# Kernel optimization log

Hardware: AMD Instinct MI355X
Metric: run time of the kernel (lower is better)

## Reference

```python
import jax, jax.numpy as jnp
import numpy as np

N = 100000   # nodes
E = 800000   # edges
IN = 64      # in_channels
H = 128      # hidden_channels (Embedding_Dimension)
K = 9        # Num_TCN clusters
EPS = 1e-15


def setup_inputs() -> dict:
    key = jax.random.key(0)
    k0, k1, k2, k3, k4 = jax.random.split(key, 5)
    x = jax.random.normal(k0, (N, IN), jnp.float32)
    edge_index = jax.random.randint(k1, (2, E), 0, N, dtype=jnp.int32)
    batch = jnp.zeros((N,), jnp.int32)  # single graph
    W1 = jax.random.normal(k2, (IN, H), jnp.float32) / np.sqrt(IN)
    b1 = jnp.zeros((H,), jnp.float32)
    Wp = jax.random.normal(k3, (H, K), jnp.float32) / np.sqrt(H)
    bp = jax.random.normal(k4, (K,), jnp.float32) * 0.01
    return {"x": x, "edge_index": edge_index, "batch": batch,
            "W1": W1, "b1": b1, "Wp": Wp, "bp": bp}


def gcn_conv(x, edge_index, W, b):
    # GCNConv: h = D^{-1/2} (A + I) D^{-1/2} (x W) + b
    n = x.shape[0]
    h = x @ W  # [N, H]
    loop = jnp.arange(n, dtype=edge_index.dtype)
    row = jnp.concatenate([edge_index[0], loop])  # source
    col = jnp.concatenate([edge_index[1], loop])  # target
    deg = jax.ops.segment_sum(jnp.ones_like(col, jnp.float32), col, n)
    dinv = jax.lax.rsqrt(jnp.maximum(deg, 1.0))  # deg >= 1 (self loops)
    norm = dinv[row] * dinv[col]  # [E+N]
    agg = jax.ops.segment_sum(norm[:, None] * h[row], col, n)  # scatter-add at targets
    return agg + b


def reference(x, edge_index, batch, W1, b1, Wp, bp):
    n = x.shape[0]
    src, dst = edge_index[0], edge_index[1]

    hx = jax.nn.relu(gcn_conv(x, edge_index, W1, b1))  # [N, H]
    s_logits = hx @ Wp + bp                             # [N, K]
    s = jax.nn.softmax(s_logits, axis=-1)

    # pooled features and adjacency: S^T X, S^T A S (A sparse via edge list)
    x_pool = s.T @ hx                                   # [K, H]
    out_adj = jnp.einsum('ek,el->kl', s[src], s[dst])   # [K, K]

    # mincut loss: -Tr(S^T A S) / Tr(S^T D S)
    mincut_num = jnp.trace(out_adj)
    deg_a = jax.ops.segment_sum(jnp.ones((src.shape[0],), jnp.float32), dst, n)
    mincut_den = jnp.sum(deg_a * jnp.sum(s * s, axis=-1))
    mc = -(mincut_num / (mincut_den + EPS))

    # orthogonality loss: || S^T S / ||S^T S||_F - I/sqrt(K) ||_F
    ss = s.T @ s
    o = jnp.linalg.norm(ss / jnp.linalg.norm(ss) - jnp.eye(K, dtype=s.dtype) / jnp.sqrt(jnp.float32(K)))

    # normalize pooled adjacency: zero diag, symmetric degree normalization
    oa = out_adj * (1.0 - jnp.eye(K, dtype=out_adj.dtype))
    d = jnp.sum(oa, axis=-1)
    dis = jax.lax.rsqrt(d + EPS)
    oa = dis[:, None] * oa * dis[None, :]

    out = jax.nn.log_softmax(x_pool[None], axis=-1)     # [1, K, H]
    return out, mc, o, s, oa[None]
```

## Files before the change

### kernel.cpp

```cpp
#include <hip/hip_runtime.h>
#include <hip/hip_bf16.h>

#define NN 100000
#define NE 800000
#define INC 64
#define HID 128
#define KC 9
#define NBKT 782
#define BCAP 2048
#define LDA 72

#define G_XP 0
#define G_OA 1152
#define G_SS 1233
#define G_DEN 1314

typedef __attribute__((ext_vector_type(8))) short bfrag;
typedef __attribute__((ext_vector_type(4))) float facc4;

__device__ __forceinline__ float atomAddG(float* p, float v) {
  return unsafeAtomicAdd(p, v);
}

__device__ __forceinline__ unsigned short bf16rn(float x) {
  unsigned u = __float_as_uint(x);
  return (unsigned short)((u + 0x7fffu + ((u >> 16) & 1u)) >> 16);
}


__global__ __launch_bounds__(256) void k_binA(const int* __restrict__ src, const int* __restrict__ dst,
                                              int* __restrict__ bcur, int* __restrict__ ebuf) {
  __shared__ int hist[NBKT];
  __shared__ int hbase[NBKT];
  int t = threadIdx.x;
  for (int b = t; b < NBKT; b += 256) hist[b] = 0;
  __syncthreads();
  int beg = blockIdx.x * 6250, end = beg + 6250;
  for (int i = beg + t; i < end; i += 256) atomicAdd(&hist[dst[i] >> 7], 1);
  __syncthreads();
  for (int b = t; b < NBKT; b += 256) {
    int h = hist[b];
    hbase[b] = h ? atomicAdd(&bcur[b], h) : 0;
    hist[b] = 0;
  }
  __syncthreads();
  for (int i = beg + t; i < end; i += 256) {
    int d = dst[i], s = src[i];
    int b = d >> 7;
    int r = atomicAdd(&hist[b], 1);
    ebuf[(size_t)b * BCAP + hbase[b] + r] = s | ((d & 127) << 17);
  }
}

__global__ __launch_bounds__(256) void k_scanb(const int* __restrict__ bcur, int* __restrict__ bbase) {
  __shared__ int sc[1024];
  int t = threadIdx.x;
  for (int i = t; i < 1024; i += 256) sc[i] = (i < NBKT) ? bcur[i] : 0;
  __syncthreads();
  for (int off = 1; off < 1024; off <<= 1) {
    int v0 = (t >= off) ? sc[t - off] : 0;
    int v1 = (t + 256 >= off) ? sc[t + 256 - off] : 0;
    int v2 = (t + 512 >= off) ? sc[t + 512 - off] : 0;
    int v3 = (t + 768 >= off) ? sc[t + 768 - off] : 0;
    __syncthreads();
    sc[t] += v0; sc[t + 256] += v1; sc[t + 512] += v2; sc[t + 768] += v3;
    __syncthreads();
  }
  for (int i = t; i < NBKT; i += 256) bbase[i] = sc[i] - bcur[i];
}

__global__ __launch_bounds__(256) void k_fillB(const int* __restrict__ bcur, const int* __restrict__ bbase,
                                               const int* __restrict__ ebuf, int* __restrict__ rowptr,
                                               int* __restrict__ degi, float* __restrict__ dinv,
                                               int* __restrict__ csr) {
  __shared__ int cnt[128], loc[128], lcur[128];
  int b = blockIdx.x;
  int t = threadIdx.x;
  if (t < 128) cnt[t] = 0;
  __syncthreads();
  int n = bcur[b];
  const int* eb = ebuf + (size_t)b * BCAP;
  for (int i = t; i < n; i += 256) atomicAdd(&cnt[eb[i] >> 17], 1);
  __syncthreads();
  if (t < 128) loc[t] = cnt[t];
  __syncthreads();
  for (int off = 1; off < 128; off <<= 1) {
    int u = (t >= off && t < 128) ? loc[t - off] : 0;
    __syncthreads();
    if (t < 128) loc[t] += u;
    __syncthreads();
  }
  int gbase = bbase[b];
  if (t < 128) {
    int node = (b << 7) + t;
    int rp = gbase + loc[t] - cnt[t];
    if (node < NN) {
      rowptr[node] = rp;
      degi[node] = cnt[t];
      dinv[node] = rsqrtf((float)cnt[t] + 1.f);
    }
    lcur[t] = rp;
  }
  __syncthreads();
  for (int i = t; i < n; i += 256) {
    int pack = eb[i];
    int s = pack & 0x1FFFF;
    int dl = pack >> 17;
    int p = atomicAdd(&lcur[dl], 1);
    csr[p] = s;
  }
}


__global__ __launch_bounds__(256) void k_gather(const int* __restrict__ rowptr, const int* __restrict__ degi,
                                                const int* __restrict__ csr, const float* __restrict__ x,
                                                const float* __restrict__ dinv, float* __restrict__ agg) {
  int t = threadIdx.x;
  int wave = t >> 6, lane = t & 63;
  int gw = blockIdx.x * 4 + wave;
  int ng = lane >> 4, c4 = lane & 15;
  int node = gw * 4 + ng;
  if (node >= NN) return;

  float dv = dinv[node];
  int base = rowptr[node];
  int cnt = degi[node];

  float4 xs = ((const float4*)(x + (size_t)node * INC))[c4];
  float dv2 = dv * dv;
  float4 acc;
  acc.x = dv2 * xs.x; acc.y = dv2 * xs.y; acc.z = dv2 * xs.z; acc.w = dv2 * xs.w;

  int j = 0;
  for (; j + 3 < cnt; j += 4) {
    int s0 = csr[base + j], s1 = csr[base + j + 1], s2 = csr[base + j + 2], s3 = csr[base + j + 3];
    float w0 = dinv[s0] * dv, w1 = dinv[s1] * dv, w2 = dinv[s2] * dv, w3 = dinv[s3] * dv;
    float4 r0 = ((const float4*)(x + (size_t)s0 * INC))[c4];
    float4 r1 = ((const float4*)(x + (size_t)s1 * INC))[c4];
    float4 r2 = ((const float4*)(x + (size_t)s2 * INC))[c4];
    float4 r3 = ((const float4*)(x + (size_t)s3 * INC))[c4];
    acc.x = fmaf(w0, r0.x, acc.x); acc.y = fmaf(w0, r0.y, acc.y);
    acc.z = fmaf(w0, r0.z, acc.z); acc.w = fmaf(w0, r0.w, acc.w);
    acc.x = fmaf(w1, r1.x, acc.x); acc.y = fmaf(w1, r1.y, acc.y);
    acc.z = fmaf(w1, r1.z, acc.z); acc.w = fmaf(w1, r1.w, acc.w);
    acc.x = fmaf(w2, r2.x, acc.x); acc.y = fmaf(w2, r2.y, acc.y);
    acc.z = fmaf(w2, r2.z, acc.z); acc.w = fmaf(w2, r2.w, acc.w);
    acc.x = fmaf(w3, r3.x, acc.x); acc.y = fmaf(w3, r3.y, acc.y);
    acc.z = fmaf(w3, r3.z, acc.z); acc.w = fmaf(w3, r3.w, acc.w);
  }
  for (; j < cnt; ++j) {
    int si = csr[base + j];
    float w = dinv[si] * dv;
    float4 r = ((const float4*)(x + (size_t)si * INC))[c4];
    acc.x = fmaf(w, r.x, acc.x); acc.y = fmaf(w, r.y, acc.y);
    acc.z = fmaf(w, r.z, acc.z); acc.w = fmaf(w, r.w, acc.w);
  }
  ((float4*)(agg + (size_t)node * INC))[c4] = acc;
}


__global__ __launch_bounds__(256, 2) void k_mlpA(const float* __restrict__ agg,
                                                 const float* __restrict__ W1, const float* __restrict__ b1,
                                                 const float* __restrict__ Wp, const float* __restrict__ bp,
                                                 float* __restrict__ s_out, float* __restrict__ s_pad,
                                                 float* __restrict__ glob) {
  __shared__ short Ahi[128 * LDA];
  __shared__ short Alo[128 * LDA];
  __shared__ short Whi[128 * LDA];
  __shared__ short Wlo[128 * LDA];

  int t = threadIdx.x;
  int nbase = blockIdx.x * 128;

#pragma unroll
  for (int j = 0; j < 8; ++j) {
    int task = t + 256 * j;
    int n = task >> 4, kq = (task & 15) * 4;
    float4 v = make_float4(0.f, 0.f, 0.f, 0.f);
    if (nbase + n < NN) v = *(const float4*)(agg + (size_t)(nbase + n) * INC + kq);
    unsigned short h0 = bf16rn(v.x), h1 = bf16rn(v.y), h2 = bf16rn(v.z), h3 = bf16rn(v.w);
    float l0f = v.x - __uint_as_float((unsigned)h0 << 16);
    float l1f = v.y - __uint_as_float((unsigned)h1 << 16);
    float l2f = v.z - __uint_as_float((unsigned)h2 << 16);
    float l3f = v.w - __uint_as_float((unsigned)h3 << 16);
    unsigned short q0 = bf16rn(l0f), q1 = bf16rn(l1f), q2 = bf16rn(l2f), q3 = bf16rn(l3f);
    *(uint2*)&Ahi[n * LDA + kq] = make_uint2((unsigned)h0 | ((unsigned)h1 << 16),
                                             (unsigned)h2 | ((unsigned)h3 << 16));
    *(uint2*)&Alo[n * LDA + kq] = make_uint2((unsigned)q0 | ((unsigned)q1 << 16),
                                             (unsigned)q2 | ((unsigned)q3 << 16));
  }
#pragma unroll
  for (int j = 0; j < 8; ++j) {
    int task = t + 256 * j;
    int c = task & 127, kq = (task >> 7) * 4;
    float v0 = W1[(kq + 0) * HID + c];
    float v1 = W1[(kq + 1) * HID + c];
    float v2 = W1[(kq + 2) * HID + c];
    float v3 = W1[(kq + 3) * HID + c];
    unsigned short h0 = bf16rn(v0), h1 = bf16rn(v1), h2 = bf16rn(v2), h3 = bf16rn(v3);
    float l0f = v0 - __uint_as_float((unsigned)h0 << 16);
    float l1f = v1 - __uint_as_float((unsigned)h1 << 16);
    float l2f = v2 - __uint_as_float((unsigned)h2 << 16);
    float l3f = v3 - __uint_as_float((unsigned)h3 << 16);
    unsigned short q0 = bf16rn(l0f), q1 = bf16rn(l1f), q2 = bf16rn(l2f), q3 = bf16rn(l3f);
    *(uint2*)&Whi[c * LDA + kq] = make_uint2((unsigned)h0 | ((unsigned)h1 << 16),
                                             (unsigned)h2 | ((unsigned)h3 << 16));
    *(uint2*)&Wlo[c * LDA + kq] = make_uint2((unsigned)q0 | ((unsigned)q1 << 16),
                                             (unsigned)q2 | ((unsigned)q3 << 16));
  }
  __syncthreads();

  int w = t >> 6, l = t & 63;
  int r0 = w * 32;
  int lrow = l & 15;
  int lk = (l >> 4) * 8;
  int rg = (l >> 4) * 4;

  facc4 acc[2][8];
#pragma unroll
  for (int mt = 0; mt < 2; ++mt)
#pragma unroll
    for (int nt = 0; nt < 8; ++nt) acc[mt][nt] = (facc4){0.f, 0.f, 0.f, 0.f};

#pragma unroll
  for (int ks = 0; ks < 2; ++ks) {
    int ko = ks * 32 + lk;
    bfrag a0h = *(const bfrag*)&Ahi[(r0 + lrow) * LDA + ko];
    bfrag a0l = *(const bfrag*)&Alo[(r0 + lrow) * LDA + ko];
    bfrag a1h = *(const bfrag*)&Ahi[(r0 + 16 + lrow) * LDA + ko];
    bfrag a1l = *(const bfrag*)&Alo[(r0 + 16 + lrow) * LDA + ko];
#pragma unroll
    for (int nt = 0; nt < 8; ++nt) {
      bfrag bh = *(const bfrag*)&Whi[(nt * 16 + lrow) * LDA + ko];
      bfrag bl = *(const bfrag*)&Wlo[(nt * 16 + lrow) * LDA + ko];
      acc[0][nt] = __builtin_amdgcn_mfma_f32_16x16x32_bf16(a0l, bh, acc[0][nt], 0, 0, 0);
      acc[0][nt] = __builtin_amdgcn_mfma_f32_16x16x32_bf16(a0h, bl, acc[0][nt], 0, 0, 0);
      acc[0][nt] = __builtin_amdgcn_mfma_f32_16x16x32_bf16(a0h, bh, acc[0][nt], 0, 0, 0);
      acc[1][nt] = __builtin_amdgcn_mfma_f32_16x16x32_bf16(a1l, bh, acc[1][nt], 0, 0, 0);
      acc[1][nt] = __builtin_amdgcn_mfma_f32_16x16x32_bf16(a1h, bl, acc[1][nt], 0, 0, 0);
      acc[1][nt] = __builtin_amdgcn_mfma_f32_16x16x32_bf16(a1h, bh, acc[1][nt], 0, 0, 0);
    }
  }

  float* pool_sh = (float*)Ahi;
  __syncthreads();
  for (int i = t; i < KC * HID; i += 256) pool_sh[i] = 0.f;
  __syncthreads();

  float pool_loc[KC][8];
#pragma unroll
  for (int q = 0; q < KC; ++q)
#pragma unroll
    for (int nt = 0; nt < 8; ++nt) pool_loc[q][nt] = 0.f;

  float bpv[KC];
#pragma unroll
  for (int q = 0; q < KC; ++q) bpv[q] = bp[q];

#pragma unroll
  for (int mt = 0; mt < 2; ++mt) {
    float plg[4][KC];
#pragma unroll
    for (int r = 0; r < 4; ++r)
#pragma unroll
      for (int q = 0; q < KC; ++q) plg[r][q] = 0.f;

#pragma unroll
    for (int nt = 0; nt < 8; ++nt) {
      int c = nt * 16 + lrow;
      float b1v = b1[c];
      float wp[KC];
#pragma unroll
      for (int q = 0; q < KC; ++q) wp[q] = Wp[c * KC + q];
#pragma unroll
      for (int r = 0; r < 4; ++r) {
        float h = fmaxf(acc[mt][nt][r] + b1v, 0.f);
        acc[mt][nt][r] = h;
#pragma unroll
        for (int q = 0; q < KC; ++q) plg[r][q] = fmaf(h, wp[q], plg[r][q]);
      }
    }
#pragma unroll
    for (int off = 1; off < 16; off <<= 1) {
#pragma unroll
      for (int r = 0; r < 4; ++r)
#pragma unroll
        for (int q = 0; q < KC; ++q)
          plg[r][q] += __shfl_xor(plg[r][q], off, 16);
    }
#pragma unroll
    for (int r = 0; r < 4; ++r) {
      int node = nbase + r0 + mt * 16 + rg + r;
      float lg[KC];
#pragma unroll
      for (int q = 0; q < KC; ++q) lg[q] = plg[r][q] + bpv[q];
      float m = lg[0];
#pragma unroll
      for (int q = 1; q < KC; ++q) m = fmaxf(m, lg[q]);
      float Z = 0.f;
#pragma unroll
      for (int q = 0; q < KC; ++q) { lg[q] = __expf(lg[q] - m); Z += lg[q]; }
      float inv = 1.0f / Z;
#pragma unroll
      for (int q = 0; q < KC; ++q) lg[q] *= inv;
      if (node < NN) {
        if (lrow < KC) s_out[(size_t)node * KC + lrow] = lg[lrow];
        if (lrow < 12) s_pad[(size_t)node * 12 + lrow] = (lrow < KC) ? lg[lrow] : 0.f;
#pragma unroll
        for (int nt = 0; nt < 8; ++nt) {
          float h = acc[mt][nt][r];
#pragma unroll
          for (int q = 0; q < KC; ++q) pool_loc[q][nt] = fmaf(lg[q], h, pool_loc[q][nt]);
        }
      }
    }
  }

#pragma unroll
  for (int q = 0; q < KC; ++q)
#pragma unroll
    for (int nt = 0; nt < 8; ++nt) {
      float v = pool_loc[q][nt];
      v += __shfl_xor(v, 16, 64);
      v += __shfl_xor(v, 32, 64);
      if ((l >> 4) == 0) atomicAdd(&pool_sh[q * HID + nt * 16 + lrow], v);
    }
  __syncthreads();
  for (int i = t; i < KC * HID; i += 256) atomAddG(&glob[G_XP + i], pool_sh[i]);
}


__global__ __launch_bounds__(256) void k_ssden(const float* __restrict__ s_pad,
                                               const int* __restrict__ degi,
                                               float* __restrict__ glob) {
  int t = threadIdx.x;
  int tid = blockIdx.x * 256 + t;
  int stride = gridDim.x * 256;

  float acc[81];
  float den = 0.f;
#pragma unroll
  for (int i = 0; i < 81; ++i) acc[i] = 0.f;

  for (int node = tid; node < NN; node += stride) {
    const float4* sn = (const float4*)(s_pad + (size_t)node * 12);
    float4 a = sn[0], b = sn[1], c = sn[2];
    float s[9] = {a.x, a.y, a.z, a.w, b.x, b.y, b.z, b.w, c.x};
    float dg = (float)degi[node];
    float nrm = 0.f;
#pragma unroll
    for (int i = 0; i < 9; ++i) nrm = fmaf(s[i], s[i], nrm);
    den = fmaf(dg, nrm, den);
#pragma unroll
    for (int i = 0; i < 9; ++i)
#pragma unroll
      for (int j = 0; j < 9; ++j) acc[i * 9 + j] = fmaf(s[i], s[j], acc[i * 9 + j]);
  }

  __shared__ float wsum[4][82];
#pragma unroll
  for (int i = 0; i < 81; ++i) {
#pragma unroll
    for (int off = 32; off > 0; off >>= 1) acc[i] += __shfl_xor(acc[i], off, 64);
  }
#pragma unroll
  for (int off = 32; off > 0; off >>= 1) den += __shfl_xor(den, off, 64);
  int wave = t >> 6, lane = t & 63;
  if (lane == 0) {
#pragma unroll
    for (int i = 0; i < 81; ++i) wsum[wave][i] = acc[i];
    wsum[wave][81] = den;
  }
  __syncthreads();
  if (t < 81) atomAddG(&glob[G_SS + t], wsum[0][t] + wsum[1][t] + wsum[2][t] + wsum[3][t]);
  if (t == 81) atomAddG(&glob[G_DEN], wsum[0][81] + wsum[1][81] + wsum[2][81] + wsum[3][81]);
}


__global__ __launch_bounds__(256) void k_adj(const int* __restrict__ rowptr, const int* __restrict__ degi,
                                             const int* __restrict__ csr, const float* __restrict__ s_pad,
                                             float* __restrict__ oa_g) {
  int t = threadIdx.x;
  int tid = blockIdx.x * blockDim.x + t;
  int stride = gridDim.x * blockDim.x;

  float acc[81];
#pragma unroll
  for (int i = 0; i < 81; ++i) acc[i] = 0.f;

  for (int node = tid; node < NN; node += stride) {
    int base = rowptr[node];
    int cnt = degi[node];
    float4 g0 = make_float4(0.f, 0.f, 0.f, 0.f);
    float4 g1 = g0;
    float g8 = 0.f;
    int j = 0;
    for (; j + 1 < cnt; j += 2) {
      int s0 = csr[base + j], s1 = csr[base + j + 1];
      const float4* p0 = (const float4*)(s_pad + (size_t)s0 * 12);
      const float4* p1 = (const float4*)(s_pad + (size_t)s1 * 12);
      float4 a0 = p0[0], b0 = p0[1], c0 = p0[2];
      float4 a1 = p1[0], b1 = p1[1], c1 = p1[2];
      g0.x += a0.x + a1.x; g0.y += a0.y + a1.y; g0.z += a0.z + a1.z; g0.w += a0.w + a1.w;
      g1.x += b0.x + b1.x; g1.y += b0.y + b1.y; g1.z += b0.z + b1.z; g1.w += b0.w + b1.w;
      g8 += c0.x + c1.x;
    }
    if (j < cnt) {
      int s0 = csr[base + j];
      const float4* p0 = (const float4*)(s_pad + (size_t)s0 * 12);
      float4 a0 = p0[0], b0 = p0[1], c0 = p0[2];
      g0.x += a0.x; g0.y += a0.y; g0.z += a0.z; g0.w += a0.w;
      g1.x += b0.x; g1.y += b0.y; g1.z += b0.z; g1.w += b0.w;
      g8 += c0.x;
    }
    const float4* sn = (const float4*)(s_pad + (size_t)node * 12);
    float4 d0 = sn[0], d1 = sn[1], d2 = sn[2];
    float gg[9] = {g0.x, g0.y, g0.z, g0.w, g1.x, g1.y, g1.z, g1.w, g8};
    float sd[9] = {d0.x, d0.y, d0.z, d0.w, d1.x, d1.y, d1.z, d1.w, d2.x};
#pragma unroll
    for (int i = 0; i < 9; ++i)
#pragma unroll
      for (int jj = 0; jj < 9; ++jj) acc[i * 9 + jj] = fmaf(gg[i], sd[jj], acc[i * 9 + jj]);
  }

  __shared__ float wsum[4][81];
#pragma unroll
  for (int i = 0; i < 81; ++i) {
#pragma unroll
    for (int off = 32; off > 0; off >>= 1) acc[i] += __shfl_xor(acc[i], off, 64);
  }
  int wave = t >> 6, lane = t & 63;
  if (lane == 0) {
#pragma unroll
    for (int i = 0; i < 81; ++i) wsum[wave][i] = acc[i];
  }
  __syncthreads();
  if (t < 81) atomAddG(&oa_g[t], wsum[0][t] + wsum[1][t] + wsum[2][t] + wsum[3][t]);
}


__global__ __launch_bounds__(128) void k_final(const float* __restrict__ glob, float* __restrict__ out) {
  const float* xp = glob + G_XP;
  const float* oa = glob + G_OA;
  const float* ssm = glob + G_SS;
  const float* den = glob + G_DEN;
  int t = threadIdx.x;
  __shared__ float red[128];

  for (int k = 0; k < 9; ++k) {
    float v = xp[k * 128 + t];
    red[t] = v;
    __syncthreads();
    for (int s2 = 64; s2 > 0; s2 >>= 1) {
      if (t < s2) red[t] = fmaxf(red[t], red[t + s2]);
      __syncthreads();
    }
    float m = red[0];
    __syncthreads();
    red[t] = expf(v - m);
    __syncthreads();
    for (int s2 = 64; s2 > 0; s2 >>= 1) {
      if (t < s2) red[t] += red[t + s2];
      __syncthreads();
    }
    float lz = logf(red[0]) + m;
    __syncthreads();
    out[k * 128 + t] = v - lz;
  }

  if (t == 0) {
    float num = 0.f;
    for (int q = 0; q < 9; ++q) num += oa[q * 9 + q];
    out[1152] = -(num / (den[0] + 1e-15f));

    float fn = 0.f;
    for (int i = 0; i < 81; ++i) fn += ssm[i] * ssm[i];
    float rfn = 1.0f / sqrtf(fn);
    float osum = 0.f;
    for (int i = 0; i < 9; ++i)
      for (int j = 0; j < 9; ++j) {
        float v = ssm[i * 9 + j] * rfn - ((i == j) ? (1.0f / 3.0f) : 0.f);
        osum += v * v;
      }
    out[1153] = sqrtf(osum);
  }

  __shared__ float dsh[9];
  if (t < 9) {
    float d = 0.f;
    for (int j = 0; j < 9; ++j)
      if (j != t) d += oa[t * 9 + j];
    dsh[t] = 1.0f / sqrtf(d + 1e-15f);
  }
  __syncthreads();
  if (t < 81) {
    int i = t / 9, j = t % 9;
    out[901154 + t] = (i == j) ? 0.f : dsh[i] * oa[t] * dsh[j];
  }
}

extern "C" void kernel_launch(void* const* d_in, const int* in_sizes, int n_in,
                              void* d_out, int out_size, void* d_ws, size_t ws_size,
                              hipStream_t stream) {
  const float* x = (const float*)d_in[0];
  const int* ei = (const int*)d_in[1];
  const float* W1 = (const float*)d_in[3];
  const float* b1 = (const float*)d_in[4];
  const float* Wp = (const float*)d_in[5];
  const float* bp = (const float*)d_in[6];
  float* out = (float*)d_out;

  float* glob = (float*)d_ws;
  int* bcur = (int*)d_ws + 1316;
  int* bbase = (int*)d_ws + 2116;
  int* rowptr = (int*)d_ws + 2944;
  int* degi = rowptr + NN;
  int* csr = degi + NN;
  float* dinv = (float*)(csr + NE);
  float* s_pad = dinv + NN;
  float* agg = s_pad + (size_t)NN * 12;
  int* ebuf = (int*)(agg + (size_t)NN * INC);

  hipMemsetAsync(d_ws, 0, (size_t)2116 * sizeof(float), stream);

  const int* src = ei;
  const int* dst = ei + NE;

  hipLaunchKernelGGL(k_binA, dim3(128), dim3(256), 0, stream, src, dst, bcur, ebuf);
  hipLaunchKernelGGL(k_scanb, dim3(1), dim3(256), 0, stream, bcur, bbase);
  hipLaunchKernelGGL(k_fillB, dim3(NBKT), dim3(256), 0, stream, bcur, bbase, ebuf,
                     rowptr, degi, dinv, csr);
  hipLaunchKernelGGL(k_gather, dim3(6250), dim3(256), 0, stream, rowptr, degi, csr, x, dinv, agg);
  hipLaunchKernelGGL(k_mlpA, dim3(NBKT), dim3(256), 0, stream, agg,
                     W1, b1, Wp, bp, out + 1154, s_pad, glob);
  hipLaunchKernelGGL(k_ssden, dim3(128), dim3(256), 0, stream, s_pad, degi, glob);
  hipLaunchKernelGGL(k_adj, dim3(1024), dim3(256), 0, stream, rowptr, degi, csr, s_pad, glob + G_OA);
  hipLaunchKernelGGL(k_final, dim3(1), dim3(128), 0, stream, glob, out);
}
```

Before: 282.0 us.

## Restructure MLP epilogue through LDS and precompute split-bf16 weights once

The W1 hi/lo bf16 split and the Wp transpose move into one extra block of the binning kernel, so each k_mlpA block no longer reconverts the weights. In k_mlpA the ReLU hidden tile is staged in shared memory. Logits are then computed per node by thread pairs, replacing the 16-lane shuffle reductions, and pooling runs per column from LDS. Pooled partials are written per block to a global buffer and reduced in k_ssden instead of using shared and global atomics. The cost is larger LDS use, which may lower occupancy, plus extra global traffic for the partials.

```diff
diff --git a/kernel.cpp b/kernel.cpp
--- a/kernel.cpp
+++ b/kernel.cpp
@@ -9,6 +9,7 @@
 #define NBKT 782
 #define BCAP 2048
 #define LDA 72
+#define LDH 132
 
 #define G_XP 0
 #define G_OA 1152
@@ -29,10 +30,33 @@
 
 
 __global__ __launch_bounds__(256) void k_binA(const int* __restrict__ src, const int* __restrict__ dst,
-                                              int* __restrict__ bcur, int* __restrict__ ebuf) {
+                                              const float* __restrict__ W1, const float* __restrict__ Wp,
+                                              int* __restrict__ bcur, int* __restrict__ ebuf,
+                                              unsigned short* __restrict__ W1Thi,
+                                              unsigned short* __restrict__ W1Tlo,
+                                              float* __restrict__ wpsT) {
+  int t = threadIdx.x;
+  if (blockIdx.x == 128) {
+    for (int i = t; i < (INC * HID) / 4; i += 256) {
+      int k = i >> 5, c4 = (i & 31) * 4;
+      float4 v = ((const float4*)W1)[i];
+      float vv[4] = {v.x, v.y, v.z, v.w};
+#pragma unroll
+      for (int j = 0; j < 4; ++j) {
+        unsigned short h = bf16rn(vv[j]);
+        float lo = vv[j] - __uint_as_float((unsigned)h << 16);
+        W1Thi[(c4 + j) * 64 + k] = h;
+        W1Tlo[(c4 + j) * 64 + k] = bf16rn(lo);
+      }
+    }
+    for (int i = t; i < KC * HID; i += 256) {
+      int q = i >> 7, c = i & 127;
+      wpsT[i] = Wp[c * KC + q];
+    }
+    return;
+  }
   __shared__ int hist[NBKT];
   __shared__ int hbase[NBKT];
-  int t = threadIdx.x;
   for (int b = t; b < NBKT; b += 256) hist[b] = 0;
   __syncthreads();
   int beg = blockIdx.x * 6250, end = beg + 6250;
@@ -160,14 +184,20 @@
 
 
 __global__ __launch_bounds__(256, 2) void k_mlpA(const float* __restrict__ agg,
-                                                 const float* __restrict__ W1, const float* __restrict__ b1,
-                                                 const float* __restrict__ Wp, const float* __restrict__ bp,
+                                                 const unsigned short* __restrict__ W1Thi,
+                                                 const unsigned short* __restrict__ W1Tlo,
+                                                 const float* __restrict__ wpsT_g,
+                                                 const float* __restrict__ b1, const float* __restrict__ bp,
                                                  float* __restrict__ s_out, float* __restrict__ s_pad,
-                                                 float* __restrict__ glob) {
-  __shared__ short Ahi[128 * LDA];
-  __shared__ short Alo[128 * LDA];
-  __shared__ short Whi[128 * LDA];
-  __shared__ short Wlo[128 * LDA];
+                                                 float* __restrict__ pool_part) {
+  __shared__ char smem[78336];
+  short* Ahi = (short*)smem;
+  short* Alo = Ahi + 128 * LDA;
+  short* Whi = Alo + 128 * LDA;
+  short* Wlo = Whi + 128 * LDA;
+  float* Hs = (float*)smem;
+  float* s_lds = Hs + 128 * LDH;
+  float* wpsT = (float*)(smem + 73728);
 
   int t = threadIdx.x;
   int nbase = blockIdx.x * 128;
@@ -192,22 +222,11 @@
 #pragma unroll
   for (int j = 0; j < 8; ++j) {
     int task = t + 256 * j;
-    int c = task & 127, kq = (task >> 7) * 4;
-    float v0 = W1[(kq + 0) * HID + c];
-    float v1 = W1[(kq + 1) * HID + c];
-    float v2 = W1[(kq + 2) * HID + c];
-    float v3 = W1[(kq + 3) * HID + c];
-    unsigned short h0 = bf16rn(v0), h1 = bf16rn(v1), h2 = bf16rn(v2), h3 = bf16rn(v3);
-    float l0f = v0 - __uint_as_float((unsigned)h0 << 16);
-    float l1f = v1 - __uint_as_float((unsigned)h1 << 16);
-    float l2f = v2 - __uint_as_float((unsigned)h2 << 16);
-    float l3f = v3 - __uint_as_float((unsigned)h3 << 16);
-    unsigned short q0 = bf16rn(l0f), q1 = bf16rn(l1f), q2 = bf16rn(l2f), q3 = bf16rn(l3f);
-    *(uint2*)&Whi[c * LDA + kq] = make_uint2((unsigned)h0 | ((unsigned)h1 << 16),
-                                             (unsigned)h2 | ((unsigned)h3 << 16));
-    *(uint2*)&Wlo[c * LDA + kq] = make_uint2((unsigned)q0 | ((unsigned)q1 << 16),
-                                             (unsigned)q2 | ((unsigned)q3 << 16));
-  }
+    int c = task >> 4, k4 = (task & 15) * 4;
+    *(uint2*)&Whi[c * LDA + k4] = *(const uint2*)&W1Thi[c * 64 + k4];
+    *(uint2*)&Wlo[c * LDA + k4] = *(const uint2*)&W1Tlo[c * 64 + k4];
+  }
+  for (int i = t; i < KC * HID; i += 256) wpsT[i] = wpsT_g[i];
   __syncthreads();
 
   int w = t >> 6, l = t & 63;
@@ -241,101 +260,132 @@
       acc[1][nt] = __builtin_amdgcn_mfma_f32_16x16x32_bf16(a1h, bh, acc[1][nt], 0, 0, 0);
     }
   }
-
-  float* pool_sh = (float*)Ahi;
-  __syncthreads();
-  for (int i = t; i < KC * HID; i += 256) pool_sh[i] = 0.f;
-  __syncthreads();
-
-  float pool_loc[KC][8];
-#pragma unroll
-  for (int q = 0; q < KC; ++q)
-#pragma unroll
-    for (int nt = 0; nt < 8; ++nt) pool_loc[q][nt] = 0.f;
-
-  float bpv[KC];
-#pragma unroll
-  for (int q = 0; q < KC; ++q) bpv[q] = bp[q];
-
-#pragma unroll
-  for (int mt = 0; mt < 2; ++mt) {
-    float plg[4][KC];
-#pragma unroll
-    for (int r = 0; r < 4; ++r)
-#pragma unroll
-      for (int q = 0; q < KC; ++q) plg[r][q] = 0.f;
-
-#pragma unroll
-    for (int nt = 0; nt < 8; ++nt) {
-      int c = nt * 16 + lrow;
-      float b1v = b1[c];
-      float wp[KC];
-#pragma unroll
-      for (int q = 0; q < KC; ++q) wp[q] = Wp[c * KC + q];
-#pragma unroll
-      for (int r = 0; r < 4; ++r) {
-        float h = fmaxf(acc[mt][nt][r] + b1v, 0.f);
-        acc[mt][nt][r] = h;
-#pragma unroll
-        for (int q = 0; q < KC; ++q) plg[r][q] = fmaf(h, wp[q], plg[r][q]);
+  __syncthreads();
+
+#pragma unroll
+  for (int nt = 0; nt < 8; ++nt) {
+    float b1v = b1[nt * 16 + lrow];
+#pragma unroll
+    for (int mt = 0; mt < 2; ++mt)
+#pragma unroll
+      for (int r = 0; r < 4; ++r)
+        Hs[(r0 + mt * 16 + rg + r) * LDH + nt * 16 + lrow] =
+            fmaxf(acc[mt][nt][r] + b1v, 0.f);
+  }
+  __syncthreads();
+
+  {
+    int node = t >> 1, half = t & 1;
+    const float4* hrow = (const float4*)(Hs + node * LDH + half * 64);
+    float4 h4[16];
+#pragma unroll
+    for (int cc = 0; cc < 16; ++cc) h4[cc] = hrow[cc];
+
+    float lg[KC];
+#pragma unroll
+    for (int q = 0; q < KC; ++q) {
+      const float4* w4 = (const float4*)(wpsT + q * HID + half * 64);
+      float s0 = 0.f, s1 = 0.f, s2 = 0.f, s3 = 0.f;
+#pragma unroll
+      for (int cc = 0; cc < 16; ++cc) {
+        float4 wv = w4[cc];
+        s0 = fmaf(h4[cc].x, wv.x, s0);
+        s1 = fmaf(h4[cc].y, wv.y, s1);
+        s2 = fmaf(h4[cc].z, wv.z, s2);
+        s3 = fmaf(h4[cc].w, wv.w, s3);
       }
-    }
-#pragma unroll
-    for (int off = 1; off < 16; off <<= 1) {
-#pragma unroll
-      for (int r = 0; r < 4; ++r)
-#pragma unroll
-        for (int q = 0; q < KC; ++q)
-          plg[r][q] += __shfl_xor(plg[r][q], off, 16);
-    }
-#pragma unroll
-    for (int r = 0; r < 4; ++r) {
-      int node = nbase + r0 + mt * 16 + rg + r;
-      float lg[KC];
-#pragma unroll
-      for (int q = 0; q < KC; ++q) lg[q] = plg[r][q] + bpv[q];
-      float m = lg[0];
-#pragma unroll
-      for (int q = 1; q < KC; ++q) m = fmaxf(m, lg[q]);
-      float Z = 0.f;
-#pragma unroll
-      for (int q = 0; q < KC; ++q) { lg[q] = __expf(lg[q] - m); Z += lg[q]; }
-      float inv = 1.0f / Z;
-#pragma unroll
-      for (int q = 0; q < KC; ++q) lg[q] *= inv;
-      if (node < NN) {
-        if (lrow < KC) s_out[(size_t)node * KC + lrow] = lg[lrow];
-        if (lrow < 12) s_pad[(size_t)node * 12 + lrow] = (lrow < KC) ? lg[lrow] : 0.f;
-#pragma unroll
-        for (int nt = 0; nt < 8; ++nt) {
-          float h = acc[mt][nt][r];
-#pragma unroll
-          for (int q = 0; q < KC; ++q) pool_loc[q][nt] = fmaf(lg[q], h, pool_loc[q][nt]);
-        }
+      lg[q] = (s0 + s1) + (s2 + s3);
+    }
+#pragma unroll
+    for (int q = 0; q < KC; ++q)
+      lg[q] = lg[q] + __shfl_xor(lg[q], 1, 64) + bp[q];
+
+    float m = lg[0];
+#pragma unroll
+    for (int q = 1; q < KC; ++q) m = fmaxf(m, lg[q]);
+    float Z = 0.f;
+#pragma unroll
+    for (int q = 0; q < KC; ++q) { lg[q] = __expf(lg[q] - m); Z += lg[q]; }
+    float inv = 1.0f / Z;
+#pragma unroll
+    for (int q = 0; q < KC; ++q) lg[q] *= inv;
+
+    float4* sl = (float4*)(s_lds + node * 12);
+    int gnode = nbase + node;
+    if (half == 0) {
+      sl[0] = make_float4(lg[0], lg[1], lg[2], lg[3]);
+      if (gnode < NN) {
+        ((float4*)(s_pad + (size_t)gnode * 12))[0] = make_float4(lg[0], lg[1], lg[2], lg[3]);
+        float* so = s_out + (size_t)gnode * KC;
+        so[0] = lg[0]; so[1] = lg[1]; so[2] = lg[2]; so[3] = lg[3]; so[4] = lg[4];
       }
-    }
-  }
-
-#pragma unroll
-  for (int q = 0; q < KC; ++q)
-#pragma unroll
-    for (int nt = 0; nt < 8; ++nt) {
-      float v = pool_loc[q][nt];
-      v += __shfl_xor(v, 16, 64);
-      v += __shfl_xor(v, 32, 64);
-      if ((l >> 4) == 0) atomicAdd(&pool_sh[q * HID + nt * 16 + lrow], v);
-    }
-  __syncthreads();
-  for (int i = t; i < KC * HID; i += 256) atomAddG(&glob[G_XP + i], pool_sh[i]);
+    } else {
+      sl[1] = make_float4(lg[4], lg[5], lg[6], lg[7]);
+      s_lds[node * 12 + 8] = lg[8];
+      if (gnode < NN) {
+        ((float4*)(s_pad + (size_t)gnode * 12))[1] = make_float4(lg[4], lg[5], lg[6], lg[7]);
+        ((float4*)(s_pad + (size_t)gnode * 12))[2] = make_float4(lg[8], 0.f, 0.f, 0.f);
+        float* so = s_out + (size_t)gnode * KC;
+        so[5] = lg[5]; so[6] = lg[6]; so[7] = lg[7]; so[8] = lg[8];
+      }
+    }
+  }
+  __syncthreads();
+
+  {
+    int c = t & 127, nh = t >> 7;
+    float pool[KC];
+#pragma unroll
+    for (int q = 0; q < KC; ++q) pool[q] = 0.f;
+    int lim = NN - nbase - nh * 64;
+    if (lim > 64) lim = 64;
+    for (int i = 0; i < lim; ++i) {
+      int node = nh * 64 + i;
+      float4 sa = *(const float4*)(s_lds + node * 12);
+      float4 sb = *(const float4*)(s_lds + node * 12 + 4);
+      float s8 = s_lds[node * 12 + 8];
+      float h = Hs[node * LDH + c];
+      pool[0] = fmaf(sa.x, h, pool[0]);
+      pool[1] = fmaf(sa.y, h, pool[1]);
+      pool[2] = fmaf(sa.z, h, pool[2]);
+      pool[3] = fmaf(sa.w, h, pool[3]);
+      pool[4] = fmaf(sb.x, h, pool[4]);
+      pool[5] = fmaf(sb.y, h, pool[5]);
+      pool[6] = fmaf(sb.z, h, pool[6]);
+      pool[7] = fmaf(sb.w, h, pool[7]);
+      pool[8] = fmaf(s8, h, pool[8]);
+    }
+    float* pp = pool_part + (size_t)(blockIdx.x * 2 + nh) * (KC * HID);
+#pragma unroll
+    for (int q = 0; q < KC; ++q) pp[q * HID + c] = pool[q];
+  }
 }
 
 
 __global__ __launch_bounds__(256) void k_ssden(const float* __restrict__ s_pad,
                                                const int* __restrict__ degi,
+                                               const float* __restrict__ pool_part,
                                                float* __restrict__ glob) {
   int t = threadIdx.x;
   int tid = blockIdx.x * 256 + t;
   int stride = gridDim.x * 256;
+
+  {
+    float a0 = 0.f, a1 = 0.f, a2 = 0.f, a3 = 0.f, a4 = 0.f;
+    for (int p = blockIdx.x; p < 2 * NBKT; p += gridDim.x) {
+      const float* row = pool_part + (size_t)p * (KC * HID);
+      a0 += row[t];
+      a1 += row[t + 256];
+      a2 += row[t + 512];
+      a3 += row[t + 768];
+      if (t < 128) a4 += row[t + 1024];
+    }
+    atomAddG(&glob[G_XP + t], a0);
+    atomAddG(&glob[G_XP + t + 256], a1);
+    atomAddG(&glob[G_XP + t + 512], a2);
+    atomAddG(&glob[G_XP + t + 768], a3);
+    if (t < 128) atomAddG(&glob[G_XP + t + 1024], a4);
+  }
 
   float acc[81];
   float den = 0.f;
@@ -520,20 +570,25 @@
   float* s_pad = dinv + NN;
   float* agg = s_pad + (size_t)NN * 12;
   int* ebuf = (int*)(agg + (size_t)NN * INC);
+  float* pool_part = (float*)(ebuf + (size_t)NBKT * BCAP);
+  unsigned short* W1Thi = (unsigned short*)(pool_part + (size_t)NBKT * 2 * (KC * HID));
+  unsigned short* W1Tlo = W1Thi + INC * HID;
+  float* wpsT = (float*)(W1Tlo + INC * HID);
 
   hipMemsetAsync(d_ws, 0, (size_t)2116 * sizeof(float), stream);
 
   const int* src = ei;
   const int* dst = ei + NE;
 
-  hipLaunchKernelGGL(k_binA, dim3(128), dim3(256), 0, stream, src, dst, bcur, ebuf);
+  hipLaunchKernelGGL(k_binA, dim3(129), dim3(256), 0, stream, src, dst, W1, Wp,
+                     bcur, ebuf, W1Thi, W1Tlo, wpsT);
   hipLaunchKernelGGL(k_scanb, dim3(1), dim3(256), 0, stream, bcur, bbase);
   hipLaunchKernelGGL(k_fillB, dim3(NBKT), dim3(256), 0, stream, bcur, bbase, ebuf,
                      rowptr, degi, dinv, csr);
   hipLaunchKernelGGL(k_gather, dim3(6250), dim3(256), 0, stream, rowptr, degi, csr, x, dinv, agg);
   hipLaunchKernelGGL(k_mlpA, dim3(NBKT), dim3(256), 0, stream, agg,
-                     W1, b1, Wp, bp, out + 1154, s_pad, glob);
-  hipLaunchKernelGGL(k_ssden, dim3(128), dim3(256), 0, stream, s_pad, degi, glob);
+                     W1Thi, W1Tlo, wpsT, b1, bp, out + 1154, s_pad, pool_part);
+  hipLaunchKernelGGL(k_ssden, dim3(128), dim3(256), 0, stream, s_pad, degi, pool_part, glob);
   hipLaunchKernelGGL(k_adj, dim3(1024), dim3(256), 0, stream, rowptr, degi, csr, s_pad, glob + G_OA);
   hipLaunchKernelGGL(k_final, dim3(1), dim3(128), 0, stream, glob, out);
 }
```

After: 249.3 us. 1.13x faster.
